# Kernel optimization log

Measured on AMD Instinct MI355X. Metric: run time of the kernel, lower is better.

## Reference

```python
import jax, jax.numpy as jnp
import numpy as np

D_MODEL = 1024
NUM_HEADS = 16
HEAD_DIM = D_MODEL // NUM_HEADS
BATCH, SEQ = 2, 2048


def setup_inputs() -> dict:
    key = jax.random.key(0)
    ks = jax.random.split(key, 5)
    scale = 1.0 / np.sqrt(D_MODEL)  # ~xavier magnitude
    x = jax.random.normal(ks[0], (BATCH, SEQ, D_MODEL), dtype=jnp.float32)
    Wq = jax.random.normal(ks[1], (D_MODEL, D_MODEL), dtype=jnp.float32) * scale
    Wk = jax.random.normal(ks[2], (D_MODEL, D_MODEL), dtype=jnp.float32) * scale
    Wv = jax.random.normal(ks[3], (D_MODEL, D_MODEL), dtype=jnp.float32) * scale
    Wo = jax.random.normal(ks[4], (D_MODEL, D_MODEL), dtype=jnp.float32) * scale
    z = jnp.zeros((D_MODEL,), dtype=jnp.float32)
    return {"x": x, "Wq": Wq, "bq": z, "Wk": Wk, "bk": z, "Wv": Wv, "bv": z, "Wo": Wo, "bo": z}


def reference(x, Wq, bq, Wk, bk, Wv, bv, Wo, bo):
    B, S, _ = x.shape
    H, Dh = NUM_HEADS, HEAD_DIM
    # torch Linear convention: y = x @ W^T + b
    q = (x @ Wq.T + bq).reshape(B, S, H, Dh)
    k = (x @ Wk.T + bk).reshape(B, S, H, Dh)
    v = (x @ Wv.T + bv).reshape(B, S, H, Dh)
    # scores: [B, H, S, S]
    scores = jnp.einsum('bqhd,bkhd->bhqk', q, k) / np.sqrt(Dh).astype(np.float32)
    attn = jax.nn.softmax(scores, axis=-1)
    out = jnp.einsum('bhqk,bkhd->bqhd', attn, v).reshape(B, S, H * Dh)
    return out @ Wo.T + bo
```

## Files before the change

### kernel.cpp

```cpp
#include <hip/hip_runtime.h>
#include <hip/hip_bf16.h>

typedef __bf16 bf16;
typedef __bf16 bf16x8 __attribute__((ext_vector_type(8)));
typedef __bf16 bf16x4 __attribute__((ext_vector_type(4)));
typedef float f32x4 __attribute__((ext_vector_type(4)));

constexpr int DM = 1024, NH = 16, DH = 64, NB = 2, SQ = 2048;
constexpr int MTOT = NB * SQ;
constexpr float QSCALE = 0.125f * 1.44269504088896f;

__device__ __forceinline__ void gld_lds16(const bf16* g, bf16* l) {
  __builtin_amdgcn_global_load_lds(
      (const __attribute__((address_space(1))) void*)g,
      (__attribute__((address_space(3))) void*)l, 16, 0, 0);
}

template <int CTRL>
__device__ __forceinline__ float fdpp(float x) {
  const int xi = __float_as_int(x);
  return __int_as_float(__builtin_amdgcn_update_dpp(xi, xi, CTRL, 0xF, 0xF, true));
}
__device__ __forceinline__ float rowsum16(float x) {
  x += fdpp<0x128>(x);
  x += fdpp<0x124>(x);
  x += fdpp<0x122>(x);
  x += fdpp<0x121>(x);
  return x;
}

__global__ __launch_bounds__(256) void cvt5(
    const float* __restrict__ s0, const float* __restrict__ s1,
    const float* __restrict__ s2, const float* __restrict__ s3,
    const float* __restrict__ s4,
    bf16* __restrict__ d0, bf16* __restrict__ d1, bf16* __restrict__ d2,
    bf16* __restrict__ d3, bf16* __restrict__ d4) {
  const float* src; bf16* dst; int n;
  switch (blockIdx.y) {
    case 0: src = s0; dst = d0; n = DM * DM; break;
    case 1: src = s1; dst = d1; n = DM * DM; break;
    case 2: src = s2; dst = d2; n = DM * DM; break;
    case 3: src = s3; dst = d3; n = DM * DM; break;
    default: src = s4; dst = d4; n = MTOT * DM; break;
  }
  const int idx = (blockIdx.x * 256 + threadIdx.x) * 4;
  if (idx < n) {
    const float4 v = *(const float4*)(src + idx);
    *(bf16x4*)(dst + idx) = (bf16x4){(bf16)v.x, (bf16)v.y, (bf16)v.z, (bf16)v.w};
  }
}

template <typename OutT>
__device__ __forceinline__ void gemm_tile(
    const bf16* __restrict__ A, const bf16* __restrict__ Bm,
    const float* __restrict__ bias, OutT* __restrict__ C,
    int rowA0, int rowB0, int N, int K, bool bias_row, float cscale,
    bf16* sA, bf16* sB) {
  const int tid = threadIdx.x;
  const int wave = tid >> 6, lane = tid & 63;
  const int wm = wave >> 1, wn = wave & 1;
  const int quad = lane >> 4, l16 = lane & 15;

  f32x4 acc[4][4];
#pragma unroll
  for (int i = 0; i < 4; i++)
#pragma unroll
    for (int j = 0; j < 4; j++) acc[i][j] = (f32x4){0.f, 0.f, 0.f, 0.f};

  const int srow = lane >> 3;
  const int scol = ((lane & 7) ^ srow) * 8;

  for (int kt = 0; kt < K; kt += 64) {
#pragma unroll
    for (int i = 0; i < 4; i++) {
      const int r = (wave * 4 + i) * 8;
      gld_lds16(A + (size_t)(rowA0 + r + srow) * K + kt + scol, &sA[r * 64]);
      gld_lds16(Bm + (size_t)(rowB0 + r + srow) * K + kt + scol, &sB[r * 64]);
    }
    __syncthreads();
#pragma unroll
    for (int kk = 0; kk < 64; kk += 32) {
      bf16x8 aF[4], bF[4];
      const int slot = (((kk >> 3) + quad) ^ (l16 & 7)) << 3;
#pragma unroll
      for (int mt = 0; mt < 4; mt++)
        aF[mt] = *(const bf16x8*)&sA[(wm * 64 + mt * 16 + l16) * 64 + slot];
#pragma unroll
      for (int nt = 0; nt < 4; nt++)
        bF[nt] = *(const bf16x8*)&sB[(wn * 64 + nt * 16 + l16) * 64 + slot];
#pragma unroll
      for (int mt = 0; mt < 4; mt++)
#pragma unroll
        for (int nt = 0; nt < 4; nt++)
          acc[mt][nt] = __builtin_amdgcn_mfma_f32_16x16x32_bf16(aF[mt], bF[nt], acc[mt][nt], 0, 0, 0);
    }
    __syncthreads();
  }

#pragma unroll
  for (int mt = 0; mt < 4; mt++) {
#pragma unroll
    for (int nt = 0; nt < 4; nt++) {
#pragma unroll
      for (int r = 0; r < 4; r++) {
        const int row = rowA0 + wm * 64 + mt * 16 + quad * 4 + r;
        const int col = rowB0 + wn * 64 + nt * 16 + l16;
        const float bb = bias_row ? bias[row] : bias[col];
        C[(size_t)row * N + col] = (OutT)((acc[mt][nt][r] + bb) * cscale);
      }
    }
  }
}

__global__ __launch_bounds__(256, 3) void qkv_gemm(
    const bf16* __restrict__ xb, const bf16* __restrict__ Wqb,
    const bf16* __restrict__ Wkb, const bf16* __restrict__ Wvb,
    const float* __restrict__ bq, const float* __restrict__ bk,
    const float* __restrict__ bv,
    bf16* __restrict__ Qw, bf16* __restrict__ Kw, bf16* __restrict__ VTw) {
  __shared__ alignas(16) bf16 sA[128 * 64];
  __shared__ alignas(16) bf16 sB[128 * 64];
  if (blockIdx.z == 0) {
    gemm_tile<bf16>(xb, Wqb, bq, Qw, blockIdx.x * 128, blockIdx.y * 128, DM, DM, false, QSCALE, sA, sB);
  } else if (blockIdx.z == 1) {
    gemm_tile<bf16>(xb, Wkb, bk, Kw, blockIdx.x * 128, blockIdx.y * 128, DM, DM, false, 1.0f, sA, sB);
  } else {
    const int id = blockIdx.y * 32 + blockIdx.x;
    gemm_tile<bf16>(Wvb, xb, bv, VTw, (id >> 5) * 128, (id & 31) * 128, MTOT, DM, true, 1.0f, sA, sB);
  }
}

__global__ __launch_bounds__(256, 3) void out_gemm(
    const bf16* __restrict__ A, const bf16* __restrict__ Bm,
    const float* __restrict__ bias, float* __restrict__ C) {
  __shared__ alignas(16) bf16 sA[128 * 64];
  __shared__ alignas(16) bf16 sB[128 * 64];
  gemm_tile<float>(A, Bm, bias, C, blockIdx.x * 128, blockIdx.y * 128, DM, DM, false, 1.0f, sA, sB);
}

__global__ __launch_bounds__(256, 2) void attn(
    const bf16* __restrict__ Q, const bf16* __restrict__ Kq,
    const bf16* __restrict__ VT, bf16* __restrict__ O) {
  __shared__ alignas(16) bf16 sQ[128 * 64];
  __shared__ alignas(16) bf16 sK[128 * 64];
  __shared__ alignas(16) bf16 sV[64 * 128];
  __shared__ alignas(16) bf16 sP[4][32 * 68];
  const int tid = threadIdx.x, wave = tid >> 6, lane = tid & 63;
  const int quad = lane >> 4, l16 = lane & 15;
  const int qt = blockIdx.x, h = blockIdx.y, b = blockIdx.z;

  const bf16* Qg = Q + (size_t)(b * SQ + qt * 128) * DM + h * DH;
  const bf16* Kg = Kq + (size_t)(b * SQ) * DM + h * DH;
  const bf16* Vg = VT + (size_t)(h * DH) * MTOT + b * SQ;

  const int srow = lane >> 3, scol = ((lane & 7) ^ srow) * 8;
  const int vrow = lane >> 4;

#pragma unroll
  for (int i = 0; i < 4; i++) {
    const int r = (wave * 4 + i) * 8;
    gld_lds16(Qg + (size_t)(r + srow) * DM + scol, &sQ[r * 64]);
  }

  float l_i[2][4];
  f32x4 o_acc[2][4];
#pragma unroll
  for (int mt = 0; mt < 2; mt++)
#pragma unroll
    for (int r = 0; r < 4; r++) l_i[mt][r] = 0.f;
#pragma unroll
  for (int mt = 0; mt < 2; mt++)
#pragma unroll
    for (int n2 = 0; n2 < 4; n2++) o_acc[mt][n2] = (f32x4){0.f, 0.f, 0.f, 0.f};

  for (int t = 0; t < 16; ++t) {
#pragma unroll
    for (int i = 0; i < 4; i++) {
      const int r = (wave * 4 + i) * 8;
      gld_lds16(Kg + (size_t)(t * 128 + r + srow) * DM + scol, &sK[r * 64]);
    }
#pragma unroll
    for (int i = 0; i < 4; i++) {
      const int r = (wave * 4 + i) * 4;
      const int vchunk = (lane & 15) ^ ((r + vrow) & 7);
      gld_lds16(Vg + (size_t)(r + vrow) * MTOT + t * 128 + vchunk * 8, &sV[r * 128]);
    }
    __syncthreads();

    f32x4 sacc[2][8];
#pragma unroll
    for (int mt = 0; mt < 2; mt++)
#pragma unroll
      for (int nt = 0; nt < 8; nt++) sacc[mt][nt] = (f32x4){0.f, 0.f, 0.f, 0.f};
#pragma unroll
    for (int kk = 0; kk < 64; kk += 32) {
      bf16x8 aF[2], bF[8];
      const int slot = (((kk >> 3) + quad) ^ (l16 & 7)) << 3;
#pragma unroll
      for (int mt = 0; mt < 2; mt++)
        aF[mt] = *(const bf16x8*)&sQ[(wave * 32 + mt * 16 + l16) * 64 + slot];
#pragma unroll
      for (int nt = 0; nt < 8; nt++)
        bF[nt] = *(const bf16x8*)&sK[(nt * 16 + l16) * 64 + slot];
#pragma unroll
      for (int mt = 0; mt < 2; mt++)
#pragma unroll
        for (int nt = 0; nt < 8; nt++)
          sacc[mt][nt] = __builtin_amdgcn_mfma_f32_16x16x32_bf16(aF[mt], bF[nt], sacc[mt][nt], 0, 0, 0);
    }

#pragma unroll
    for (int half = 0; half < 2; half++) {
#pragma unroll
      for (int mt = 0; mt < 2; mt++) {
#pragma unroll
        for (int r = 0; r < 4; r++) {
#pragma unroll
          for (int nt4 = 0; nt4 < 4; nt4++) {
            const float p = __builtin_amdgcn_exp2f(sacc[mt][half * 4 + nt4][r]);
            l_i[mt][r] += p;
            sP[wave][(mt * 16 + quad * 4 + r) * 68 + nt4 * 16 + l16] = (bf16)p;
          }
        }
      }
#pragma unroll
      for (int kk = 0; kk < 64; kk += 32) {
        bf16x8 aF[2], bF[4];
#pragma unroll
        for (int mt = 0; mt < 2; mt++) {
          union { bf16x8 v8; bf16x4 v4[2]; } u;
          u.v4[0] = *(const bf16x4*)&sP[wave][(mt * 16 + l16) * 68 + kk + quad * 8];
          u.v4[1] = *(const bf16x4*)&sP[wave][(mt * 16 + l16) * 68 + kk + quad * 8 + 4];
          aF[mt] = u.v8;
        }
#pragma unroll
        for (int n2 = 0; n2 < 4; n2++) {
          const int ch = ((half * 64 + kk) >> 3) + quad;
          bF[n2] = *(const bf16x8*)&sV[(n2 * 16 + l16) * 128 + ((ch ^ (l16 & 7)) << 3)];
        }
#pragma unroll
        for (int mt = 0; mt < 2; mt++)
#pragma unroll
          for (int n2 = 0; n2 < 4; n2++)
            o_acc[mt][n2] = __builtin_amdgcn_mfma_f32_16x16x32_bf16(aF[mt], bF[n2], o_acc[mt][n2], 0, 0, 0);
      }
    }
    __syncthreads();
  }

#pragma unroll
  for (int mt = 0; mt < 2; mt++) {
#pragma unroll
    for (int r = 0; r < 4; r++) {
      const float inv = 1.0f / rowsum16(l_i[mt][r]);
      const int row = qt * 128 + wave * 32 + mt * 16 + quad * 4 + r;
#pragma unroll
      for (int n2 = 0; n2 < 4; n2++) {
        const int col = n2 * 16 + l16;
        O[(size_t)(b * SQ + row) * DM + h * DH + col] = (bf16)(o_acc[mt][n2][r] * inv);
      }
    }
  }
}

extern "C" void kernel_launch(void* const* d_in, const int* in_sizes, int n_in,
                              void* d_out, int out_size, void* d_ws, size_t ws_size,
                              hipStream_t stream) {
  const float* x  = (const float*)d_in[0];
  const float* Wq = (const float*)d_in[1];
  const float* bq = (const float*)d_in[2];
  const float* Wk = (const float*)d_in[3];
  const float* bk = (const float*)d_in[4];
  const float* Wv = (const float*)d_in[5];
  const float* bv = (const float*)d_in[6];
  const float* Wo = (const float*)d_in[7];
  const float* bo = (const float*)d_in[8];
  float* out = (float*)d_out;

  bf16* ws   = (bf16*)d_ws;
  bf16* xb   = ws;
  bf16* Wqb  = ws + (size_t)MTOT * DM;
  bf16* Wkb  = Wqb + (size_t)DM * DM;
  bf16* Wvb  = Wkb + (size_t)DM * DM;
  bf16* Wob  = Wvb + (size_t)DM * DM;
  bf16* Qw   = Wob + (size_t)DM * DM;
  bf16* Kw   = Qw + (size_t)MTOT * DM;
  bf16* VTw  = Kw + (size_t)MTOT * DM;
  bf16* Cw   = VTw + (size_t)MTOT * DM;

  const dim3 blk(256);
  cvt5<<<dim3(MTOT * DM / 1024, 5), blk, 0, stream>>>(Wq, Wk, Wv, Wo, x,
                                                      Wqb, Wkb, Wvb, Wob, xb);
  qkv_gemm<<<dim3(32, 8, 3), blk, 0, stream>>>(xb, Wqb, Wkb, Wvb, bq, bk, bv, Qw, Kw, VTw);
  attn<<<dim3(SQ / 128, NH, NB), blk, 0, stream>>>(Qw, Kw, VTw, Cw);
  out_gemm<<<dim3(MTOT / 128, DM / 128), blk, 0, stream>>>(Cw, Wob, bo, out);
}
```

Baseline: 199.9 us.

## Transpose QK^T MFMA, keep Q in registers, swizzle P tile, reorder attention grid

The attention kernel now loads Q fragments straight into registers instead of staging them in LDS, and swaps the MFMA operands so S^T is produced. Each lane then holds a full key-row chunk, which allows packed bf16x4 stores of P into an XOR-swizzled, unpadded LDS tile and replaces the DPP row reduction with shuffles plus an LDS exchange. The smaller LDS footprint allows occupancy 3 for attention, while the GEMMs drop to 2. The grid is reordered so blocks sharing a head and batch run adjacently, which may improve K/V cache reuse. The s_waitcnt before reading lbuf stands in for a barrier, which is only safe if the cross-lane LDS exchange is ordered within the wave.

```diff
diff --git a/kernel.cpp b/kernel.cpp
--- a/kernel.cpp
+++ b/kernel.cpp
@@ -14,19 +14,6 @@
   __builtin_amdgcn_global_load_lds(
       (const __attribute__((address_space(1))) void*)g,
       (__attribute__((address_space(3))) void*)l, 16, 0, 0);
-}
-
-template <int CTRL>
-__device__ __forceinline__ float fdpp(float x) {
-  const int xi = __float_as_int(x);
-  return __int_as_float(__builtin_amdgcn_update_dpp(xi, xi, CTRL, 0xF, 0xF, true));
-}
-__device__ __forceinline__ float rowsum16(float x) {
-  x += fdpp<0x128>(x);
-  x += fdpp<0x124>(x);
-  x += fdpp<0x122>(x);
-  x += fdpp<0x121>(x);
-  return x;
 }
 
 __global__ __launch_bounds__(256) void cvt5(
@@ -112,7 +99,7 @@
   }
 }
 
-__global__ __launch_bounds__(256, 3) void qkv_gemm(
+__global__ __launch_bounds__(256, 2) void qkv_gemm(
     const bf16* __restrict__ xb, const bf16* __restrict__ Wqb,
     const bf16* __restrict__ Wkb, const bf16* __restrict__ Wvb,
     const float* __restrict__ bq, const float* __restrict__ bk,
@@ -130,7 +117,7 @@
   }
 }
 
-__global__ __launch_bounds__(256, 3) void out_gemm(
+__global__ __launch_bounds__(256, 2) void out_gemm(
     const bf16* __restrict__ A, const bf16* __restrict__ Bm,
     const float* __restrict__ bias, float* __restrict__ C) {
   __shared__ alignas(16) bf16 sA[128 * 64];
@@ -138,16 +125,16 @@
   gemm_tile<float>(A, Bm, bias, C, blockIdx.x * 128, blockIdx.y * 128, DM, DM, false, 1.0f, sA, sB);
 }
 
-__global__ __launch_bounds__(256, 2) void attn(
+__global__ __launch_bounds__(256, 3) void attn(
     const bf16* __restrict__ Q, const bf16* __restrict__ Kq,
     const bf16* __restrict__ VT, bf16* __restrict__ O) {
-  __shared__ alignas(16) bf16 sQ[128 * 64];
   __shared__ alignas(16) bf16 sK[128 * 64];
   __shared__ alignas(16) bf16 sV[64 * 128];
-  __shared__ alignas(16) bf16 sP[4][32 * 68];
+  __shared__ alignas(16) bf16 sP[4][32 * 64];
   const int tid = threadIdx.x, wave = tid >> 6, lane = tid & 63;
   const int quad = lane >> 4, l16 = lane & 15;
-  const int qt = blockIdx.x, h = blockIdx.y, b = blockIdx.z;
+  const int hb = blockIdx.x, qt = blockIdx.y;
+  const int h = hb & 15, b = hb >> 4;
 
   const bf16* Qg = Q + (size_t)(b * SQ + qt * 128) * DM + h * DH;
   const bf16* Kg = Kq + (size_t)(b * SQ) * DM + h * DH;
@@ -156,18 +143,16 @@
   const int srow = lane >> 3, scol = ((lane & 7) ^ srow) * 8;
   const int vrow = lane >> 4;
 
-#pragma unroll
-  for (int i = 0; i < 4; i++) {
-    const int r = (wave * 4 + i) * 8;
-    gld_lds16(Qg + (size_t)(r + srow) * DM + scol, &sQ[r * 64]);
-  }
-
-  float l_i[2][4];
+  bf16x8 qF[2][2];
+#pragma unroll
+  for (int mt = 0; mt < 2; mt++)
+#pragma unroll
+    for (int kkh = 0; kkh < 2; kkh++)
+      qF[mt][kkh] = *(const bf16x8*)(Qg + (size_t)(wave * 32 + mt * 16 + l16) * DM +
+                                     kkh * 32 + quad * 8);
+
+  float l_i[2] = {0.f, 0.f};
   f32x4 o_acc[2][4];
-#pragma unroll
-  for (int mt = 0; mt < 2; mt++)
-#pragma unroll
-    for (int r = 0; r < 4; r++) l_i[mt][r] = 0.f;
 #pragma unroll
   for (int mt = 0; mt < 2; mt++)
 #pragma unroll
@@ -194,65 +179,78 @@
       for (int nt = 0; nt < 8; nt++) sacc[mt][nt] = (f32x4){0.f, 0.f, 0.f, 0.f};
 #pragma unroll
     for (int kk = 0; kk < 64; kk += 32) {
-      bf16x8 aF[2], bF[8];
+      bf16x8 kF[8];
       const int slot = (((kk >> 3) + quad) ^ (l16 & 7)) << 3;
 #pragma unroll
+      for (int nt = 0; nt < 8; nt++)
+        kF[nt] = *(const bf16x8*)&sK[(nt * 16 + l16) * 64 + slot];
+#pragma unroll
       for (int mt = 0; mt < 2; mt++)
-        aF[mt] = *(const bf16x8*)&sQ[(wave * 32 + mt * 16 + l16) * 64 + slot];
-#pragma unroll
-      for (int nt = 0; nt < 8; nt++)
-        bF[nt] = *(const bf16x8*)&sK[(nt * 16 + l16) * 64 + slot];
-#pragma unroll
-      for (int mt = 0; mt < 2; mt++)
 #pragma unroll
         for (int nt = 0; nt < 8; nt++)
-          sacc[mt][nt] = __builtin_amdgcn_mfma_f32_16x16x32_bf16(aF[mt], bF[nt], sacc[mt][nt], 0, 0, 0);
+          sacc[mt][nt] = __builtin_amdgcn_mfma_f32_16x16x32_bf16(kF[nt], qF[mt][kk >> 5],
+                                                                 sacc[mt][nt], 0, 0, 0);
     }
 
 #pragma unroll
     for (int half = 0; half < 2; half++) {
 #pragma unroll
       for (int mt = 0; mt < 2; mt++) {
-#pragma unroll
-        for (int r = 0; r < 4; r++) {
-#pragma unroll
-          for (int nt4 = 0; nt4 < 4; nt4++) {
-            const float p = __builtin_amdgcn_exp2f(sacc[mt][half * 4 + nt4][r]);
-            l_i[mt][r] += p;
-            sP[wave][(mt * 16 + quad * 4 + r) * 68 + nt4 * 16 + l16] = (bf16)p;
+        const int row = mt * 16 + l16;
+#pragma unroll
+        for (int nt4 = 0; nt4 < 4; nt4++) {
+          const f32x4 s = sacc[mt][half * 4 + nt4];
+          bf16x4 pk;
+#pragma unroll
+          for (int r = 0; r < 4; r++) {
+            const float p = __builtin_amdgcn_exp2f(s[r]);
+            l_i[mt] += p;
+            pk[r] = (bf16)p;
           }
+          const int c = 2 * nt4 + (quad >> 1);
+          *(bf16x4*)&sP[wave][row * 64 + ((c ^ (row & 7)) << 3) + (quad & 1) * 4] = pk;
         }
       }
 #pragma unroll
       for (int kk = 0; kk < 64; kk += 32) {
-        bf16x8 aF[2], bF[4];
+        bf16x8 pF[2], vF[4];
 #pragma unroll
         for (int mt = 0; mt < 2; mt++) {
-          union { bf16x8 v8; bf16x4 v4[2]; } u;
-          u.v4[0] = *(const bf16x4*)&sP[wave][(mt * 16 + l16) * 68 + kk + quad * 8];
-          u.v4[1] = *(const bf16x4*)&sP[wave][(mt * 16 + l16) * 68 + kk + quad * 8 + 4];
-          aF[mt] = u.v8;
+          const int row = mt * 16 + l16;
+          const int c = (kk >> 3) + quad;
+          pF[mt] = *(const bf16x8*)&sP[wave][row * 64 + ((c ^ (row & 7)) << 3)];
         }
 #pragma unroll
         for (int n2 = 0; n2 < 4; n2++) {
           const int ch = ((half * 64 + kk) >> 3) + quad;
-          bF[n2] = *(const bf16x8*)&sV[(n2 * 16 + l16) * 128 + ((ch ^ (l16 & 7)) << 3)];
+          vF[n2] = *(const bf16x8*)&sV[(n2 * 16 + l16) * 128 + ((ch ^ (l16 & 7)) << 3)];
         }
 #pragma unroll
         for (int mt = 0; mt < 2; mt++)
 #pragma unroll
           for (int n2 = 0; n2 < 4; n2++)
-            o_acc[mt][n2] = __builtin_amdgcn_mfma_f32_16x16x32_bf16(aF[mt], bF[n2], o_acc[mt][n2], 0, 0, 0);
-      }
-    }
-    __syncthreads();
-  }
-
+            o_acc[mt][n2] = __builtin_amdgcn_mfma_f32_16x16x32_bf16(pF[mt], vF[n2],
+                                                                    o_acc[mt][n2], 0, 0, 0);
+      }
+    }
+    __syncthreads();
+  }
+
+  float* lbuf = (float*)&sP[wave][0];
 #pragma unroll
   for (int mt = 0; mt < 2; mt++) {
+    float v = l_i[mt];
+    v += __shfl_xor(v, 16);
+    v += __shfl_xor(v, 32);
+    if (quad == 0) lbuf[mt * 16 + l16] = v;
+  }
+  __builtin_amdgcn_s_waitcnt(0);
+#pragma unroll
+  for (int mt = 0; mt < 2; mt++) {
+    const f32x4 lv = *(const f32x4*)&lbuf[mt * 16 + quad * 4];
 #pragma unroll
     for (int r = 0; r < 4; r++) {
-      const float inv = 1.0f / rowsum16(l_i[mt][r]);
+      const float inv = 1.0f / lv[r];
       const int row = qt * 128 + wave * 32 + mt * 16 + quad * 4 + r;
 #pragma unroll
       for (int n2 = 0; n2 < 4; n2++) {
@@ -292,6 +290,6 @@
   cvt5<<<dim3(MTOT * DM / 1024, 5), blk, 0, stream>>>(Wq, Wk, Wv, Wo, x,
                                                       Wqb, Wkb, Wvb, Wob, xb);
   qkv_gemm<<<dim3(32, 8, 3), blk, 0, stream>>>(xb, Wqb, Wkb, Wvb, bq, bk, bv, Qw, Kw, VTw);
-  attn<<<dim3(SQ / 128, NH, NB), blk, 0, stream>>>(Qw, Kw, VTw, Cw);
+  attn<<<dim3(NH * NB, SQ / 128), blk, 0, stream>>>(Qw, Kw, VTw, Cw);
   out_gemm<<<dim3(MTOT / 128, DM / 128), blk, 0, stream>>>(Cw, Wob, bo, out);
 }
```

New measurement: 192.2 us. 3.8% less time.
